# Kernel tuning notes

Measured on AMD Instinct MI355X. Metric: run time of the kernel, lower is better.

## Reference

```python
import jax, jax.numpy as jnp
import numpy as np

NEG_SLOPE = 0.2

def setup_inputs() -> dict:
    key = jax.random.key(0)
    k1, k2, k3, k4, k5 = jax.random.split(key, 5)
    B, N, Fin, Fout, H = 4, 2048, 256, 128, 4
    h = jax.random.normal(k1, (B, N, Fin), dtype=jnp.float32)
    adj = jax.random.randint(k2, (N, N), 0, 2, dtype=jnp.int32)
    W_w = jax.random.normal(k3, (Fout, Fin), dtype=jnp.float32) * (1.414 / np.sqrt(Fin))
    W_b = jax.random.normal(k4, (Fout,), dtype=jnp.float32) * 0.01
    attn_w = jax.random.normal(k5, (H, 2 * Fout), dtype=jnp.float32) * (1.414 / np.sqrt(2 * Fout))
    return {"h": h, "adj": adj, "W_w": W_w, "W_b": W_b, "attn_w": attn_w}

def reference(h, adj, W_w, W_b, attn_w):
    Fout = W_w.shape[0]
    # Wh: [B, N, Fout]
    Wh = jnp.einsum('bnf,of->bno', h, W_w) + W_b
    a_left = attn_w[:, :Fout]   # [H, Fout]
    a_right = attn_w[:, Fout:]  # [H, Fout]
    e_left = jnp.einsum('bno,ho->bhn', Wh, a_left)   # [B, H, N]
    e_right = jnp.einsum('bno,ho->bhn', Wh, a_right)  # [B, H, N]
    # additive broadcast score: [B, H, N, N]
    e = e_left[:, :, :, None] + e_right[:, :, None, :]
    e = jnp.where(e > 0, e, NEG_SLOPE * e)  # LeakyReLU(0.2)
    mask = (adj == 0)[None, None, :, :]     # [1,1,N,N] broadcast over B,H
    e = jnp.where(mask, -jnp.inf, e)
    attn = jax.nn.softmax(e, axis=-1)
    attn = jnp.where(jnp.isnan(attn), 0.0, attn)
    # h_prime: [B, H, N, Fout]
    h_prime = jnp.einsum('bhij,bjo->bhio', attn, Wh)
    out = jnp.mean(h_prime, axis=1)
    return jax.nn.relu(out)
```

## Files before the change

### kernel.cpp

```cpp
#include <hip/hip_runtime.h>
#include <stdint.h>

#define BB 4
#define NN 2048
#define FIN 256
#define FOUT 128
#define NH 4
#define NEG_SLOPE 0.2f

typedef short bf16x8 __attribute__((ext_vector_type(8)));
typedef unsigned short u16x8 __attribute__((ext_vector_type(8)));
typedef float f32x4 __attribute__((ext_vector_type(4)));
typedef unsigned long long u64;

__device__ inline float b2f(unsigned short u) {
    union { unsigned int i; float f; } x; x.i = ((unsigned int)u) << 16; return x.f;
}
__device__ inline unsigned short f2b(float f) {
    union { float f; unsigned int i; } x; x.f = f;
    unsigned int r = x.i + 0x7fffu + ((x.i >> 16) & 1u);
    return (unsigned short)(r >> 16);
}
__device__ inline unsigned short f2b_fast(float f) {
    union { float f; unsigned int i; } x; x.f = f;
    return (unsigned short)((x.i + 0x8000u) >> 16);
}
union F16U { unsigned short u; _Float16 h; };
__device__ inline float f16lo(unsigned int v) { F16U x; x.u = (unsigned short)(v & 0xffffu); return (float)x.h; }
__device__ inline float f16hi(unsigned int v) { F16U x; x.u = (unsigned short)(v >> 16); return (float)x.h; }
__device__ inline unsigned int packf16(float a, float b) {
    F16U x, y; x.h = (_Float16)a; y.h = (_Float16)b;
    return (unsigned int)x.u | ((unsigned int)y.u << 16);
}

__global__ __launch_bounds__(256) void kcvt_w(const float* __restrict__ Ww,
                                              unsigned short* __restrict__ Whi,
                                              unsigned short* __restrict__ Wlo) {
    int idx = blockIdx.x * 256 + threadIdx.x;
    float v = Ww[idx];
    unsigned short hb = f2b(v);
    Whi[idx] = hb;
    Wlo[idx] = f2b(v - b2f(hb));
}

__global__ __launch_bounds__(256) void k1_wh(
    const float* __restrict__ h, const unsigned short* __restrict__ Whi,
    const unsigned short* __restrict__ Wlo, const float* __restrict__ Wb,
    const float* __restrict__ attw, unsigned short* __restrict__ WhT,
    float2* __restrict__ ELpair, unsigned int* __restrict__ ERpk,
    unsigned int* __restrict__ ERpk2) {
    __shared__ unsigned short Ahi[16][264];
    __shared__ unsigned short Alo[16][264];
    __shared__ float whs[16][132];
    int t = threadIdx.x;
    int b = blockIdx.x >> 7;
    int n0 = (blockIdx.x & 127) * 16;
    {
        int r = t >> 4, c = (t & 15) * 16;
        const float* hp = h + ((size_t)(b * NN + n0 + r)) * FIN + c;
        u16x8 hi0, hi1, lo0, lo1;
        #pragma unroll
        for (int q = 0; q < 4; ++q) {
            float4 v = *(const float4*)(hp + q * 4);
            float vv[4] = {v.x, v.y, v.z, v.w};
            #pragma unroll
            for (int e = 0; e < 4; ++e) {
                int idx = q * 4 + e;
                unsigned short hb = f2b(vv[e]);
                unsigned short lb = f2b(vv[e] - b2f(hb));
                if (idx < 8) { hi0[idx] = (short)hb; lo0[idx] = (short)lb; }
                else         { hi1[idx - 8] = (short)hb; lo1[idx - 8] = (short)lb; }
            }
        }
        *(u16x8*)&Ahi[r][c] = *(u16x8*)&hi0;
        *(u16x8*)&Ahi[r][c + 8] = *(u16x8*)&hi1;
        *(u16x8*)&Alo[r][c] = *(u16x8*)&lo0;
        *(u16x8*)&Alo[r][c + 8] = *(u16x8*)&lo1;
    }
    __syncthreads();
    int lane = t & 63, wv = t >> 6;
    int m = lane & 15, quad = lane >> 4;
    int o0 = wv * 32;
    f32x4 acc0 = {0.f, 0.f, 0.f, 0.f}, acc1 = {0.f, 0.f, 0.f, 0.f};
    const unsigned short* wh0 = Whi + (size_t)(o0 + m) * FIN;
    const unsigned short* wl0 = Wlo + (size_t)(o0 + m) * FIN;
    const unsigned short* wh1 = Whi + (size_t)(o0 + 16 + m) * FIN;
    const unsigned short* wl1 = Wlo + (size_t)(o0 + 16 + m) * FIN;
    #pragma unroll
    for (int ks = 0; ks < 8; ++ks) {
        int ko = ks * 32 + quad * 8;
        bf16x8 ahi = *(bf16x8*)&Ahi[m][ko];
        bf16x8 alo = *(bf16x8*)&Alo[m][ko];
        bf16x8 bh0 = *(const bf16x8*)(wh0 + ko);
        bf16x8 bl0 = *(const bf16x8*)(wl0 + ko);
        bf16x8 bh1 = *(const bf16x8*)(wh1 + ko);
        bf16x8 bl1 = *(const bf16x8*)(wl1 + ko);
        acc0 = __builtin_amdgcn_mfma_f32_16x16x32_bf16(ahi, bh0, acc0, 0, 0, 0);
        acc0 = __builtin_amdgcn_mfma_f32_16x16x32_bf16(ahi, bl0, acc0, 0, 0, 0);
        acc0 = __builtin_amdgcn_mfma_f32_16x16x32_bf16(alo, bh0, acc0, 0, 0, 0);
        acc1 = __builtin_amdgcn_mfma_f32_16x16x32_bf16(ahi, bh1, acc1, 0, 0, 0);
        acc1 = __builtin_amdgcn_mfma_f32_16x16x32_bf16(ahi, bl1, acc1, 0, 0, 0);
        acc1 = __builtin_amdgcn_mfma_f32_16x16x32_bf16(alo, bh1, acc1, 0, 0, 0);
    }
    float bias0 = Wb[o0 + m], bias1 = Wb[o0 + 16 + m];
    #pragma unroll
    for (int reg = 0; reg < 4; ++reg) {
        int row = quad * 4 + reg;
        whs[row][o0 + m] = acc0[reg] + bias0;
        whs[row][o0 + 16 + m] = acc1[reg] + bias1;
    }
    __syncthreads();
    {
        int o = t >> 1, half = t & 1;
        u16x8 v8;
        #pragma unroll
        for (int r = 0; r < 8; ++r) v8[r] = (short)f2b(whs[half * 8 + r][o]);
        *(u16x8*)(WhT + (size_t)(b * FOUT + o) * NN + n0 + half * 8) = v8;
    }
    {
        int outi = t >> 1, half = t & 1;
        int i = outi >> 3, d = outi & 7, hh = d & 3, side = d >> 2;
        const float* arow = attw + hh * (2 * FOUT) + side * FOUT + half * 64;
        float s = 0.f;
        #pragma unroll 8
        for (int k = 0; k < 64; ++k) s = fmaf(whs[i][half * 64 + k], arow[k], s);
        s += __shfl_xor(s, 1);
        if (half == 0) {
            float p = __expf(s), n = __expf(NEG_SLOPE * s);
            int bh = b * NH + hh;
            if (side == 0) {
                ELpair[(size_t)bh * NN + n0 + i] = make_float2(p, n);
            } else {
                unsigned int pk = packf16(p, n);
                ERpk[((size_t)b * NN + n0 + i) * NH + hh] = pk;
                ERpk2[(size_t)bh * NN + n0 + i] = pk;
            }
        }
    }
}

__global__ __launch_bounds__(256) void kpack_fused(
    const int* __restrict__ adj, const float2* __restrict__ ELpair,
    const unsigned int* __restrict__ ERpk2, u64* __restrict__ mask,
    float* __restrict__ ELSC) {
    __shared__ float red[16][4];
    int i = blockIdx.x;
    int t = threadIdx.x, lane = t & 63, wv = t >> 6;
    int nz[8];
    #pragma unroll
    for (int k = 0; k < 8; ++k) {
        int a = adj[(size_t)i * NN + k * 256 + t];
        nz[k] = (a != 0);
        u64 bal = __ballot(nz[k] != 0);
        if (lane == 0) mask[i * 32 + k * 4 + wv] = bal;
    }
    float s[16];
    #pragma unroll
    for (int bh = 0; bh < 16; ++bh) {
        float2 el = ELpair[(size_t)bh * NN + i];
        float acc = 0.f;
        #pragma unroll
        for (int k = 0; k < 8; ++k) {
            unsigned int er = ERpk2[(size_t)bh * NN + k * 256 + t];
            float p = fmaxf(el.x * f16lo(er), el.y * f16hi(er));
            acc += nz[k] ? p : 0.f;
        }
        s[bh] = acc;
    }
    #pragma unroll
    for (int bh = 0; bh < 16; ++bh) {
        float v = s[bh];
        #pragma unroll
        for (int off = 32; off; off >>= 1) v += __shfl_xor(v, off);
        if (lane == 0) red[bh][wv] = v;
    }
    __syncthreads();
    if (t < 16) {
        float tot = red[t][0] + red[t][1] + red[t][2] + red[t][3];
        float iv = (tot > 0.f) ? 1.f / (4.f * tot) : 0.f;
        float2 el = ELpair[(size_t)t * NN + i];
        int bb = t >> 2, hh = t & 3;
        float* dst = ELSC + ((size_t)bb * NN + i) * 8 + hh * 2;
        dst[0] = el.x * iv;
        dst[1] = el.y * iv;
    }
}

__global__ __launch_bounds__(512, 2) void k2b_mfma(
    const unsigned short* __restrict__ WhT, const unsigned int* __restrict__ ERpk,
    const float* __restrict__ ELSC, const u64* __restrict__ mask,
    float* __restrict__ P) {
    __shared__ unsigned short wt[64][264];
    __shared__ u64 mws[64][16];
    __shared__ float elsc_s[64][8];
    int t = threadIdx.x;
    int b = blockIdx.y, i0 = blockIdx.x * 64, jhalf = blockIdx.z;
    int lane = t & 63, wv = t >> 6;
    int m = lane & 15, quad = lane >> 4;
    if (t < 128) {
        ((float4*)elsc_s)[t] = *(const float4*)(ELSC + ((size_t)b * NN + i0) * 8 + t * 4);
    }
    {
        int r = t >> 3, wp = (t & 7) * 2;
        *(ulonglong2*)&mws[r][wp] =
            *(const ulonglong2*)(mask + (size_t)(i0 + r) * 32 + jhalf * 16 + wp);
    }
    int r0 = wv * 8;
    int o0 = wv * 16;
    const unsigned short* bp = WhT + (size_t)(b * FOUT + o0 + m) * NN + jhalf * 1024;
    f32x4 acc[4];
    #pragma unroll
    for (int k = 0; k < 4; ++k) acc[k] = (f32x4){0.f, 0.f, 0.f, 0.f};

    for (int ch = 0; ch < 4; ++ch) {
        int j0 = ch * 256;
        __syncthreads();
        bf16x8 bfr[8];
        #pragma unroll
        for (int ks = 0; ks < 8; ++ks)
            bfr[ks] = *(const bf16x8*)(bp + j0 + ks * 32 + quad * 8);
        float erp[4][4], ern[4][4];
        #pragma unroll
        for (int q = 0; q < 4; ++q) {
            int jg = jhalf * 1024 + j0 + q * 64 + lane;
            uint4 er4 = *(const uint4*)(ERpk + ((size_t)b * NN + jg) * 4);
            erp[q][0] = f16lo(er4.x); ern[q][0] = f16hi(er4.x);
            erp[q][1] = f16lo(er4.y); ern[q][1] = f16hi(er4.y);
            erp[q][2] = f16lo(er4.z); ern[q][2] = f16hi(er4.z);
            erp[q][3] = f16lo(er4.w); ern[q][3] = f16hi(er4.w);
        }
        #pragma unroll
        for (int r = 0; r < 8; ++r) {
            int ir = r0 + r;
            float4 c0 = *(float4*)&elsc_s[ir][0];
            float4 c1 = *(float4*)&elsc_s[ir][4];
            u64 mw0 = mws[ir][ch * 4 + 0];
            u64 mw1 = mws[ir][ch * 4 + 1];
            u64 mw2 = mws[ir][ch * 4 + 2];
            u64 mw3 = mws[ir][ch * 4 + 3];
            u64 mwq[4] = {mw0, mw1, mw2, mw3};
            #pragma unroll
            for (int q = 0; q < 4; ++q) {
                float p = fmaxf(c0.x * erp[q][0], c0.y * ern[q][0]);
                p += fmaxf(c0.z * erp[q][1], c0.w * ern[q][1]);
                p += fmaxf(c1.x * erp[q][2], c1.y * ern[q][2]);
                p += fmaxf(c1.z * erp[q][3], c1.w * ern[q][3]);
                wt[ir][q * 64 + lane] = ((mwq[q] >> lane) & 1ull) ? f2b_fast(p) : 0;
            }
        }
        __syncthreads();
        #pragma unroll
        for (int isub = 0; isub < 4; ++isub) {
            #pragma unroll
            for (int ks = 0; ks < 8; ++ks) {
                bf16x8 a = *(bf16x8*)&wt[isub * 16 + m][ks * 32 + quad * 8];
                acc[isub] = __builtin_amdgcn_mfma_f32_16x16x32_bf16(a, bfr[ks], acc[isub], 0, 0, 0);
            }
        }
    }
    float* pb = P + (((size_t)jhalf * BB + b) * NN + i0) * FOUT;
    #pragma unroll
    for (int isub = 0; isub < 4; ++isub) {
        #pragma unroll
        for (int reg = 0; reg < 4; ++reg) {
            int row = isub * 16 + quad * 4 + reg;
            pb[(size_t)row * FOUT + o0 + m] = acc[isub][reg];
        }
    }
}

__global__ __launch_bounds__(256) void k3_relu(const float* __restrict__ P,
                                               float* __restrict__ out) {
    int idx = blockIdx.x * 256 + threadIdx.x;
    float4 a = ((const float4*)P)[idx];
    float4 c = ((const float4*)P)[idx + (BB * NN * FOUT / 4)];
    a.x = fmaxf(a.x + c.x, 0.f); a.y = fmaxf(a.y + c.y, 0.f);
    a.z = fmaxf(a.z + c.z, 0.f); a.w = fmaxf(a.w + c.w, 0.f);
    ((float4*)out)[idx] = a;
}

extern "C" void kernel_launch(void* const* d_in, const int* in_sizes, int n_in,
                              void* d_out, int out_size, void* d_ws, size_t ws_size,
                              hipStream_t stream) {
    const float* h    = (const float*)d_in[0];
    const int* adj    = (const int*)d_in[1];
    const float* Ww   = (const float*)d_in[2];
    const float* Wb   = (const float*)d_in[3];
    const float* attw = (const float*)d_in[4];
    float* out = (float*)d_out;
    char* ws = (char*)d_ws;
    unsigned short* Whi = (unsigned short*)(ws);
    unsigned short* Wlo = (unsigned short*)(ws + 65536);
    unsigned short* WhT = (unsigned short*)(ws + 131072);
    float2*       ELpair = (float2*)(ws + 2228224);
    unsigned int* ERpk   = (unsigned int*)(ws + 2490368);
    unsigned int* ERpk2  = (unsigned int*)(ws + 2621440);
    float*        ELSC   = (float*)(ws + 2752512);
    u64*          mask   = (u64*)(ws + 3014656);
    float*        P      = (float*)(ws + 3538944);

    kcvt_w<<<dim3(128), dim3(256), 0, stream>>>(Ww, Whi, Wlo);
    k1_wh<<<dim3(BB * NN / 16), dim3(256), 0, stream>>>(h, Whi, Wlo, Wb, attw,
                                                        WhT, ELpair, ERpk, ERpk2);
    kpack_fused<<<dim3(NN), dim3(256), 0, stream>>>(adj, ELpair, ERpk2, mask, ELSC);
    k2b_mfma<<<dim3(NN / 64, BB, 2), dim3(512), 0, stream>>>(WhT, ERpk, ELSC, mask, P);
    k3_relu<<<dim3(BB * NN * FOUT / 1024), dim3(256), 0, stream>>>(P, out);
}
```

Measured before the change: 155.4 us.

## Split adjacency packing from softmax-denominator stats and compute stats from bitmask

The fused pack+stat kernel becomes two kernels. k_pack only packs adjacency into bitmasks. kstat computes the per-row softmax denominators from the bitmask and the row-major ERpk layout, with each wave handling 4 rows across all heads and one block per 16 rows per batch. The duplicate ERpk2 buffer and its writes are removed, and each ER load is reused across 4 rows and 4 heads. This trades one extra kernel launch for less redundant global traffic and better reuse in the statistics pass.

```diff
diff --git a/kernel.cpp b/kernel.cpp
--- a/kernel.cpp
+++ b/kernel.cpp
@@ -47,8 +47,7 @@
     const float* __restrict__ h, const unsigned short* __restrict__ Whi,
     const unsigned short* __restrict__ Wlo, const float* __restrict__ Wb,
     const float* __restrict__ attw, unsigned short* __restrict__ WhT,
-    float2* __restrict__ ELpair, unsigned int* __restrict__ ERpk,
-    unsigned int* __restrict__ ERpk2) {
+    float2* __restrict__ ELpair, unsigned int* __restrict__ ERpk) {
     __shared__ unsigned short Ahi[16][264];
     __shared__ unsigned short Alo[16][264];
     __shared__ float whs[16][132];
@@ -127,62 +126,83 @@
         s += __shfl_xor(s, 1);
         if (half == 0) {
             float p = __expf(s), n = __expf(NEG_SLOPE * s);
-            int bh = b * NH + hh;
             if (side == 0) {
-                ELpair[(size_t)bh * NN + n0 + i] = make_float2(p, n);
+                ELpair[(size_t)(b * NH + hh) * NN + n0 + i] = make_float2(p, n);
             } else {
-                unsigned int pk = packf16(p, n);
-                ERpk[((size_t)b * NN + n0 + i) * NH + hh] = pk;
-                ERpk2[(size_t)bh * NN + n0 + i] = pk;
+                ERpk[((size_t)b * NN + n0 + i) * NH + hh] = packf16(p, n);
             }
         }
     }
 }
 
-__global__ __launch_bounds__(256) void kpack_fused(
-    const int* __restrict__ adj, const float2* __restrict__ ELpair,
-    const unsigned int* __restrict__ ERpk2, u64* __restrict__ mask,
-    float* __restrict__ ELSC) {
-    __shared__ float red[16][4];
-    int i = blockIdx.x;
+__global__ __launch_bounds__(256) void k_pack(const int* __restrict__ adj,
+                                              u64* __restrict__ mask) {
+    int row = blockIdx.x;
+    int wave = threadIdx.x >> 6, lane = threadIdx.x & 63;
+    #pragma unroll
+    for (int it = 0; it < 8; ++it) {
+        int w = it * 4 + wave;
+        int j = w * 64 + lane;
+        u64 m = __ballot(adj[(size_t)row * NN + j] != 0);
+        if (lane == 0) mask[row * 32 + w] = m;
+    }
+}
+
+__global__ __launch_bounds__(256) void kstat(
+    const unsigned int* __restrict__ ERpk, const float2* __restrict__ ELpair,
+    const u64* __restrict__ mask, float* __restrict__ ELSC) {
     int t = threadIdx.x, lane = t & 63, wv = t >> 6;
-    int nz[8];
-    #pragma unroll
-    for (int k = 0; k < 8; ++k) {
-        int a = adj[(size_t)i * NN + k * 256 + t];
-        nz[k] = (a != 0);
-        u64 bal = __ballot(nz[k] != 0);
-        if (lane == 0) mask[i * 32 + k * 4 + wv] = bal;
-    }
-    float s[16];
-    #pragma unroll
-    for (int bh = 0; bh < 16; ++bh) {
-        float2 el = ELpair[(size_t)bh * NN + i];
-        float acc = 0.f;
-        #pragma unroll
-        for (int k = 0; k < 8; ++k) {
-            unsigned int er = ERpk2[(size_t)bh * NN + k * 256 + t];
-            float p = fmaxf(el.x * f16lo(er), el.y * f16hi(er));
-            acc += nz[k] ? p : 0.f;
-        }
-        s[bh] = acc;
-    }
-    #pragma unroll
-    for (int bh = 0; bh < 16; ++bh) {
-        float v = s[bh];
-        #pragma unroll
-        for (int off = 32; off; off >>= 1) v += __shfl_xor(v, off);
-        if (lane == 0) red[bh][wv] = v;
-    }
-    __syncthreads();
-    if (t < 16) {
-        float tot = red[t][0] + red[t][1] + red[t][2] + red[t][3];
+    int b = blockIdx.y;
+    int i0 = blockIdx.x * 16 + wv * 4;
+    float elp[4][4], eln[4][4];
+    #pragma unroll
+    for (int r = 0; r < 4; ++r)
+        #pragma unroll
+        for (int hh = 0; hh < 4; ++hh) {
+            float2 e2 = ELpair[(size_t)(b * NH + hh) * NN + i0 + r];
+            elp[r][hh] = e2.x; eln[r][hh] = e2.y;
+        }
+    float acc[4][4];
+    #pragma unroll
+    for (int r = 0; r < 4; ++r)
+        #pragma unroll
+        for (int hh = 0; hh < 4; ++hh) acc[r][hh] = 0.f;
+
+    const uint4* erb = (const uint4*)(ERpk + (size_t)b * NN * NH);
+    #pragma unroll 2
+    for (int jc = 0; jc < 32; ++jc) {
+        uint4 er4 = erb[jc * 64 + lane];
+        float erp0 = f16lo(er4.x), ern0 = f16hi(er4.x);
+        float erp1 = f16lo(er4.y), ern1 = f16hi(er4.y);
+        float erp2 = f16lo(er4.z), ern2 = f16hi(er4.z);
+        float erp3 = f16lo(er4.w), ern3 = f16hi(er4.w);
+        #pragma unroll
+        for (int r = 0; r < 4; ++r) {
+            u64 mw = mask[(size_t)(i0 + r) * 32 + jc];
+            bool bit = (mw >> lane) & 1ull;
+            acc[r][0] += bit ? fmaxf(elp[r][0] * erp0, eln[r][0] * ern0) : 0.f;
+            acc[r][1] += bit ? fmaxf(elp[r][1] * erp1, eln[r][1] * ern1) : 0.f;
+            acc[r][2] += bit ? fmaxf(elp[r][2] * erp2, eln[r][2] * ern2) : 0.f;
+            acc[r][3] += bit ? fmaxf(elp[r][3] * erp3, eln[r][3] * ern3) : 0.f;
+        }
+    }
+    #pragma unroll
+    for (int r = 0; r < 4; ++r)
+        #pragma unroll
+        for (int hh = 0; hh < 4; ++hh) {
+            float v = acc[r][hh];
+            #pragma unroll
+            for (int off = 32; off; off >>= 1) v += __shfl_xor(v, off);
+            acc[r][hh] = v;
+        }
+    if (lane < 16) {
+        int r = lane >> 2, hh = lane & 3;
+        float tot = acc[r][hh];
         float iv = (tot > 0.f) ? 1.f / (4.f * tot) : 0.f;
-        float2 el = ELpair[(size_t)t * NN + i];
-        int bb = t >> 2, hh = t & 3;
-        float* dst = ELSC + ((size_t)bb * NN + i) * 8 + hh * 2;
-        dst[0] = el.x * iv;
-        dst[1] = el.y * iv;
+        float2 e2 = ELpair[(size_t)(b * NH + hh) * NN + i0 + r];
+        float* dst = ELSC + ((size_t)b * NN + i0 + r) * 8 + hh * 2;
+        dst[0] = e2.x * iv;
+        dst[1] = e2.y * iv;
     }
 }
 
@@ -234,11 +254,8 @@
             int ir = r0 + r;
             float4 c0 = *(float4*)&elsc_s[ir][0];
             float4 c1 = *(float4*)&elsc_s[ir][4];
-            u64 mw0 = mws[ir][ch * 4 + 0];
-            u64 mw1 = mws[ir][ch * 4 + 1];
-            u64 mw2 = mws[ir][ch * 4 + 2];
-            u64 mw3 = mws[ir][ch * 4 + 3];
-            u64 mwq[4] = {mw0, mw1, mw2, mw3};
+            u64 mwq[4] = {mws[ir][ch * 4 + 0], mws[ir][ch * 4 + 1],
+                          mws[ir][ch * 4 + 2], mws[ir][ch * 4 + 3]};
             #pragma unroll
             for (int q = 0; q < 4; ++q) {
                 float p = fmaxf(c0.x * erp[q][0], c0.y * ern[q][0]);
@@ -294,15 +311,15 @@
     unsigned short* WhT = (unsigned short*)(ws + 131072);
     float2*       ELpair = (float2*)(ws + 2228224);
     unsigned int* ERpk   = (unsigned int*)(ws + 2490368);
-    unsigned int* ERpk2  = (unsigned int*)(ws + 2621440);
-    float*        ELSC   = (float*)(ws + 2752512);
-    u64*          mask   = (u64*)(ws + 3014656);
-    float*        P      = (float*)(ws + 3538944);
+    float*        ELSC   = (float*)(ws + 2621440);
+    u64*          mask   = (u64*)(ws + 2883584);
+    float*        P      = (float*)(ws + 3407872);
 
     kcvt_w<<<dim3(128), dim3(256), 0, stream>>>(Ww, Whi, Wlo);
     k1_wh<<<dim3(BB * NN / 16), dim3(256), 0, stream>>>(h, Whi, Wlo, Wb, attw,
-                                                        WhT, ELpair, ERpk, ERpk2);
-    kpack_fused<<<dim3(NN), dim3(256), 0, stream>>>(adj, ELpair, ERpk2, mask, ELSC);
+                                                        WhT, ELpair, ERpk);
+    k_pack<<<dim3(NN), dim3(256), 0, stream>>>(adj, mask);
+    kstat<<<dim3(NN / 16, BB), dim3(256), 0, stream>>>(ERpk, ELpair, mask, ELSC);
     k2b_mfma<<<dim3(NN / 64, BB, 2), dim3(512), 0, stream>>>(WhT, ERpk, ELSC, mask, P);
     k3_relu<<<dim3(BB * NN * FOUT / 1024), dim3(256), 0, stream>>>(P, out);
 }
```

New measurement: 167.8 us. +8.0%, slower.
